# Performance work log

Measured on AMD Instinct MI355X. Metric: run time of the kernel, lower is better.

Reference implementation:

```python
import jax, jax.numpy as jnp
import numpy as np

B, T, D, H, G = 256, 1024, 32, 64, 4 * 64  # batch, seq, input, hidden, gates


def setup_inputs() -> dict:
    key = jax.random.key(0)
    ks = jax.random.split(key, 12)
    s = 1.0 / np.sqrt(H)  # PyTorch LSTM default init scale
    return {
        "x": jax.random.normal(ks[0], (B, T, D), dtype=jnp.float32),
        "w_ih_l0": jax.random.normal(ks[1], (G, D), dtype=jnp.float32) * s,
        "w_hh_l0": jax.random.normal(ks[2], (G, H), dtype=jnp.float32) * s,
        "b_ih_l0": jax.random.normal(ks[3], (G,), dtype=jnp.float32) * s,
        "b_hh_l0": jax.random.normal(ks[4], (G,), dtype=jnp.float32) * s,
        "w_ih_l1": jax.random.normal(ks[5], (G, H), dtype=jnp.float32) * s,
        "w_hh_l1": jax.random.normal(ks[6], (G, H), dtype=jnp.float32) * s,
        "b_ih_l1": jax.random.normal(ks[7], (G,), dtype=jnp.float32) * s,
        "b_hh_l1": jax.random.normal(ks[8], (G,), dtype=jnp.float32) * s,
        "w_fc": jax.random.normal(ks[9], (1, H), dtype=jnp.float32) * s,
        "b_fc": jax.random.normal(ks[10], (1,), dtype=jnp.float32) * s,
    }


def _lstm_layer(x, w_ih, w_hh, b_ih, b_hh):
    """x: [B, T, Din] -> h_seq [B, T, H]. PyTorch gate order (i, f, g, o)."""
    # Precompute input contribution for all timesteps in one GEMM.
    gx = jnp.einsum('btd,gd->btg', x, w_ih) + b_ih + b_hh  # [B, T, 4H]
    gx = jnp.swapaxes(gx, 0, 1)  # [T, B, 4H] for scan over time
    h0 = jnp.zeros((x.shape[0], H), dtype=x.dtype)
    c0 = jnp.zeros((x.shape[0], H), dtype=x.dtype)

    def step(carry, g_t):
        h, c = carry
        g = g_t + h @ w_hh.T  # [B, 4H]
        i, f, gg, o = jnp.split(g, 4, axis=-1)
        i = jax.nn.sigmoid(i)
        f = jax.nn.sigmoid(f)
        gg = jnp.tanh(gg)
        o = jax.nn.sigmoid(o)
        c = f * c + i * gg
        h = o * jnp.tanh(c)
        return (h, c), h

    _, h_seq = jax.lax.scan(step, (h0, c0), gx)  # h_seq: [T, B, H]
    return jnp.swapaxes(h_seq, 0, 1)  # [B, T, H]


def reference(x, w_ih_l0, w_hh_l0, b_ih_l0, b_hh_l0,
              w_ih_l1, w_hh_l1, b_ih_l1, b_hh_l1, w_fc, b_fc):
    h1 = _lstm_layer(x, w_ih_l0, w_hh_l0, b_ih_l0, b_hh_l0)
    h2 = _lstm_layer(h1, w_ih_l1, w_hh_l1, b_ih_l1, b_hh_l1)
    last = h2[:, -1, :]  # [B, H]
    logits = last @ w_fc.T + b_fc  # [B, 1]
    return jax.nn.sigmoid(logits)
```

## Files before the change

kernel.cpp:

```cpp
#include <hip/hip_runtime.h>

#define TT 1024
#define DD 32
#define HH 64

typedef __fp16 h2 __attribute__((ext_vector_type(2)));

__device__ __forceinline__ float fsig(float x) {
    float e = __builtin_amdgcn_exp2f(-1.4426950408889634f * x);
    return __builtin_amdgcn_rcpf(1.0f + e);
}

template<int CTRL>
__device__ __forceinline__ float fdpp(float x) {
    int r = __builtin_amdgcn_mov_dpp(__builtin_bit_cast(int, x), CTRL, 0xf, 0xf, true);
    return __builtin_bit_cast(float, r);
}

struct __attribute__((aligned(16))) H16 { h2 p[8]; };

__device__ __forceinline__ void cvt4rtn(float4 f, h2* d) {
    d[0] = (h2){(__fp16)f.x, (__fp16)f.y};
    d[1] = (h2){(__fp16)f.z, (__fp16)f.w};
}

__global__ __launch_bounds__(512, 1) void lstm2_dot2(
    const float* __restrict__ x,
    const float* __restrict__ w_ih_l0, const float* __restrict__ w_hh_l0,
    const float* __restrict__ b_ih_l0, const float* __restrict__ b_hh_l0,
    const float* __restrict__ w_ih_l1, const float* __restrict__ w_hh_l1,
    const float* __restrict__ b_ih_l1, const float* __restrict__ b_hh_l1,
    const float* __restrict__ w_fc,   const float* __restrict__ b_fc,
    float* __restrict__ out)
{
    const int b    = blockIdx.x;
    const int tid  = threadIdx.x;
    const bool isL1 = tid < 256;
    const int gtid = tid & 255;
    const int q    = gtid & 3;
    const int j    = gtid >> 2;
    const int g    = q * 64 + j;

    __shared__ __attribute__((aligned(32))) __fp16 h1s[2][HH];
    __shared__ __attribute__((aligned(32))) __fp16 h2sB[2][HH];
    if (tid < HH) {
        h1s[0][tid] = (__fp16)0.f; h1s[1][tid] = (__fp16)0.f;
        h2sB[0][tid] = (__fp16)0.f; h2sB[1][tid] = (__fp16)0.f;
    }

    const float kk = (q == 2) ? -2.885390081777927f : -1.4426950408889634f;
    const float aa = (q == 2) ? 2.0f : 1.0f;
    const float bb = (q == 2) ? -1.0f : 0.0f;

    h2 wh[64];
    float bias;
    if (isL1) {
        #pragma unroll
        for (int m = 0; m < 4; ++m) {
            const float4* pih = (const float4*)(w_ih_l0 + (m*64 + j)*DD + q*8);
            cvt4rtn(pih[0], &wh[m*12 + 0]);
            cvt4rtn(pih[1], &wh[m*12 + 2]);
            const float4* phh = (const float4*)(w_hh_l0 + (m*64 + j)*HH + q*16);
            cvt4rtn(phh[0], &wh[m*12 + 4]);
            cvt4rtn(phh[1], &wh[m*12 + 6]);
            cvt4rtn(phh[2], &wh[m*12 + 8]);
            cvt4rtn(phh[3], &wh[m*12 + 10]);
        }
        bias = b_ih_l0[g] + b_hh_l0[g];
    } else {
        #pragma unroll
        for (int m = 0; m < 4; ++m) {
            const float4* pih = (const float4*)(w_ih_l1 + (m*64 + j)*HH + q*16);
            cvt4rtn(pih[0], &wh[m*16 + 0]);
            cvt4rtn(pih[1], &wh[m*16 + 2]);
            cvt4rtn(pih[2], &wh[m*16 + 4]);
            cvt4rtn(pih[3], &wh[m*16 + 6]);
            const float4* phh = (const float4*)(w_hh_l1 + (m*64 + j)*HH + q*16);
            cvt4rtn(phh[0], &wh[m*16 + 8]);
            cvt4rtn(phh[1], &wh[m*16 + 10]);
            cvt4rtn(phh[2], &wh[m*16 + 12]);
            cvt4rtn(phh[3], &wh[m*16 + 14]);
        }
        bias = b_ih_l1[g] + b_hh_l1[g];
    }

    float c = 0.0f;

    const float* xbase = x + (size_t)b * TT * DD + q * 8;
    h2 xh[4];
    if (isL1) {
        const float4* xp = (const float4*)xbase;
        float4 a0 = xp[0], a1 = xp[1];
        xh[0] = __builtin_amdgcn_cvt_pkrtz(a0.x, a0.y);
        xh[1] = __builtin_amdgcn_cvt_pkrtz(a0.z, a0.w);
        xh[2] = __builtin_amdgcn_cvt_pkrtz(a1.x, a1.y);
        xh[3] = __builtin_amdgcn_cvt_pkrtz(a1.z, a1.w);
    }

    __syncthreads();

    for (int t = 0; t <= TT; ++t) {
        const int prev = (t + 1) & 1;
        const int cur  = t & 1;
        if (isL1) {
            if (t < TT) {
                const int tn = (t + 1 < TT) ? (t + 1) : t;
                const float4* xp = (const float4*)(xbase + (size_t)tn * DD);
                float4 n0 = xp[0], n1 = xp[1];

                H16 hq = *(const H16*)&h1s[prev][q*16];

                float P[4];
                #pragma unroll
                for (int m = 0; m < 4; ++m) {
                    float s = 0.0f;
                    #pragma unroll
                    for (int k = 0; k < 4; ++k)
                        s = __builtin_amdgcn_fdot2(wh[m*12 + k], xh[k], s, false);
                    #pragma unroll
                    for (int k = 0; k < 8; ++k)
                        s = __builtin_amdgcn_fdot2(wh[m*12 + 4 + k], hq.p[k], s, false);
                    P[m] = s;
                }

                float t0 = P[0] + fdpp<0xB1>(P[0]);
                float t1 = P[1] + fdpp<0xB1>(P[1]);
                float t2 = P[2] + fdpp<0xB1>(P[2]);
                float t3 = P[3] + fdpp<0xB1>(P[3]);
                float Alo = (q & 1) ? t1 : t0;
                float Ahi = (q & 1) ? t3 : t2;
                float ulo = Alo + fdpp<0x4E>(Alo);
                float uhi = Ahi + fdpp<0x4E>(Ahi);
                float S = ((q & 2) ? uhi : ulo) + bias;

                float e = __builtin_amdgcn_exp2f(kk * S);
                float v = aa * __builtin_amdgcn_rcpf(1.0f + e) + bb;

                float gi = fdpp<0x00>(v);
                float gf = fdpp<0x55>(v);
                float gg = fdpp<0xAA>(v);
                float go = fdpp<0xFF>(v);
                c = gf * c + gi * gg;
                float e2 = __builtin_amdgcn_exp2f(-2.885390081777927f * c);
                float th = 2.0f * __builtin_amdgcn_rcpf(1.0f + e2) - 1.0f;
                float hv = go * th;
                if (q == 0) h1s[cur][j] = (__fp16)hv;

                xh[0] = __builtin_amdgcn_cvt_pkrtz(n0.x, n0.y);
                xh[1] = __builtin_amdgcn_cvt_pkrtz(n0.z, n0.w);
                xh[2] = __builtin_amdgcn_cvt_pkrtz(n1.x, n1.y);
                xh[3] = __builtin_amdgcn_cvt_pkrtz(n1.z, n1.w);
            }
        } else {
            if (t > 0) {
                H16 a1 = *(const H16*)&h1s[prev][q*16];
                H16 a2 = *(const H16*)&h2sB[prev][q*16];

                float P[4];
                #pragma unroll
                for (int m = 0; m < 4; ++m) {
                    float s = 0.0f;
                    #pragma unroll
                    for (int k = 0; k < 8; ++k)
                        s = __builtin_amdgcn_fdot2(wh[m*16 + k], a1.p[k], s, false);
                    #pragma unroll
                    for (int k = 0; k < 8; ++k)
                        s = __builtin_amdgcn_fdot2(wh[m*16 + 8 + k], a2.p[k], s, false);
                    P[m] = s;
                }

                float t0 = P[0] + fdpp<0xB1>(P[0]);
                float t1 = P[1] + fdpp<0xB1>(P[1]);
                float t2 = P[2] + fdpp<0xB1>(P[2]);
                float t3 = P[3] + fdpp<0xB1>(P[3]);
                float Alo = (q & 1) ? t1 : t0;
                float Ahi = (q & 1) ? t3 : t2;
                float ulo = Alo + fdpp<0x4E>(Alo);
                float uhi = Ahi + fdpp<0x4E>(Ahi);
                float S = ((q & 2) ? uhi : ulo) + bias;

                float e = __builtin_amdgcn_exp2f(kk * S);
                float v = aa * __builtin_amdgcn_rcpf(1.0f + e) + bb;

                float gi = fdpp<0x00>(v);
                float gf = fdpp<0x55>(v);
                float gg = fdpp<0xAA>(v);
                float go = fdpp<0xFF>(v);
                c = gf * c + gi * gg;
                float e2 = __builtin_amdgcn_exp2f(-2.885390081777927f * c);
                float th = 2.0f * __builtin_amdgcn_rcpf(1.0f + e2) - 1.0f;
                float hv = go * th;
                if (q == 0) h2sB[cur][j] = (__fp16)hv;
            }
        }
        __syncthreads();
    }

    if (tid < HH) {
        float v = (float)h2sB[0][tid] * w_fc[tid];
        #pragma unroll
        for (int off = 32; off > 0; off >>= 1) v += __shfl_down(v, off);
        if (tid == 0) out[b] = fsig(v + b_fc[0]);
    }
}

extern "C" void kernel_launch(void* const* d_in, const int* in_sizes, int n_in,
                              void* d_out, int out_size, void* d_ws, size_t ws_size,
                              hipStream_t stream) {
    lstm2_dot2<<<dim3(256), dim3(512), 0, stream>>>(
        (const float*)d_in[0],
        (const float*)d_in[1], (const float*)d_in[2],
        (const float*)d_in[3], (const float*)d_in[4],
        (const float*)d_in[5], (const float*)d_in[6],
        (const float*)d_in[7], (const float*)d_in[8],
        (const float*)d_in[9], (const float*)d_in[10],
        (float*)d_out);
}
```

Baseline: 571.0 us.

## Split each gate dot product across eight lanes with 1024-thread blocks

Blocks grow from 512 to 1024 threads, and each hidden unit now uses eight lanes instead of four, each covering half the previous K-chunk. This halves the serial fdot2 chain per timestep in both layers and the per-thread weight registers. An extra ds_swizzle xor-4 step finishes the cross-lane reduction. The aim is to shorten per-step latency in the recurrence, at the cost of a swizzle through the LDS crossbar and a 16-wave barrier every step.

```diff
diff --git a/kernel.cpp b/kernel.cpp
--- a/kernel.cpp
+++ b/kernel.cpp
@@ -17,14 +17,20 @@
     return __builtin_bit_cast(float, r);
 }
 
-struct __attribute__((aligned(16))) H16 { h2 p[8]; };
-
-__device__ __forceinline__ void cvt4rtn(float4 f, h2* d) {
-    d[0] = (h2){(__fp16)f.x, (__fp16)f.y};
-    d[1] = (h2){(__fp16)f.z, (__fp16)f.w};
-}
-
-__global__ __launch_bounds__(512, 1) void lstm2_dot2(
+__device__ __forceinline__ float fswz4(float x) {
+    int r = __builtin_amdgcn_ds_swizzle(__builtin_bit_cast(int, x), 0x101F);
+    return __builtin_bit_cast(float, r);
+}
+
+struct __attribute__((aligned(16))) H8 { h2 p[4]; };
+
+__device__ __forceinline__ void cvt4(float4 f, h2* d) {
+    d[0] = __builtin_amdgcn_cvt_pkrtz(f.x, f.y);
+    d[1] = __builtin_amdgcn_cvt_pkrtz(f.z, f.w);
+}
+
+__global__ __launch_bounds__(1024) __attribute__((amdgpu_waves_per_eu(4, 4)))
+void lstm2_w16(
     const float* __restrict__ x,
     const float* __restrict__ w_ih_l0, const float* __restrict__ w_hh_l0,
     const float* __restrict__ b_ih_l0, const float* __restrict__ b_hh_l0,
@@ -35,11 +41,11 @@
 {
     const int b    = blockIdx.x;
     const int tid  = threadIdx.x;
-    const bool isL1 = tid < 256;
-    const int gtid = tid & 255;
-    const int q    = gtid & 3;
-    const int j    = gtid >> 2;
-    const int g    = q * 64 + j;
+    const bool isL1 = tid < 512;
+    const int gtid = tid & 511;
+    const int c_ch = gtid & 7;
+    const int j    = gtid >> 3;
+    const int ga   = (c_ch & 3) * 64 + j;
 
     __shared__ __attribute__((aligned(32))) __fp16 h1s[2][HH];
     __shared__ __attribute__((aligned(32))) __fp16 h2sB[2][HH];
@@ -48,53 +54,43 @@
         h2sB[0][tid] = (__fp16)0.f; h2sB[1][tid] = (__fp16)0.f;
     }
 
-    const float kk = (q == 2) ? -2.885390081777927f : -1.4426950408889634f;
-    const float aa = (q == 2) ? 2.0f : 1.0f;
-    const float bb = (q == 2) ? -1.0f : 0.0f;
-
-    h2 wh[64];
+    const float kk = ((c_ch & 3) == 2) ? -2.885390081777927f : -1.4426950408889634f;
+    const float aa = ((c_ch & 3) == 2) ? 2.0f : 1.0f;
+    const float bb = ((c_ch & 3) == 2) ? -1.0f : 0.0f;
+
+    h2 wh[32];
     float bias;
     if (isL1) {
         #pragma unroll
         for (int m = 0; m < 4; ++m) {
-            const float4* pih = (const float4*)(w_ih_l0 + (m*64 + j)*DD + q*8);
-            cvt4rtn(pih[0], &wh[m*12 + 0]);
-            cvt4rtn(pih[1], &wh[m*12 + 2]);
-            const float4* phh = (const float4*)(w_hh_l0 + (m*64 + j)*HH + q*16);
-            cvt4rtn(phh[0], &wh[m*12 + 4]);
-            cvt4rtn(phh[1], &wh[m*12 + 6]);
-            cvt4rtn(phh[2], &wh[m*12 + 8]);
-            cvt4rtn(phh[3], &wh[m*12 + 10]);
+            float4 fih = *(const float4*)(w_ih_l0 + (m*64 + j)*DD + c_ch*4);
+            cvt4(fih, &wh[m*6 + 0]);
+            const float4* phh = (const float4*)(w_hh_l0 + (m*64 + j)*HH + c_ch*8);
+            cvt4(phh[0], &wh[m*6 + 2]);
+            cvt4(phh[1], &wh[m*6 + 4]);
         }
-        bias = b_ih_l0[g] + b_hh_l0[g];
+        bias = b_ih_l0[ga] + b_hh_l0[ga];
     } else {
         #pragma unroll
         for (int m = 0; m < 4; ++m) {
-            const float4* pih = (const float4*)(w_ih_l1 + (m*64 + j)*HH + q*16);
-            cvt4rtn(pih[0], &wh[m*16 + 0]);
-            cvt4rtn(pih[1], &wh[m*16 + 2]);
-            cvt4rtn(pih[2], &wh[m*16 + 4]);
-            cvt4rtn(pih[3], &wh[m*16 + 6]);
-            const float4* phh = (const float4*)(w_hh_l1 + (m*64 + j)*HH + q*16);
-            cvt4rtn(phh[0], &wh[m*16 + 8]);
-            cvt4rtn(phh[1], &wh[m*16 + 10]);
-            cvt4rtn(phh[2], &wh[m*16 + 12]);
-            cvt4rtn(phh[3], &wh[m*16 + 14]);
+            const float4* pih = (const float4*)(w_ih_l1 + (m*64 + j)*HH + c_ch*8);
+            cvt4(pih[0], &wh[m*8 + 0]);
+            cvt4(pih[1], &wh[m*8 + 2]);
+            const float4* phh = (const float4*)(w_hh_l1 + (m*64 + j)*HH + c_ch*8);
+            cvt4(phh[0], &wh[m*8 + 4]);
+            cvt4(phh[1], &wh[m*8 + 6]);
         }
-        bias = b_ih_l1[g] + b_hh_l1[g];
-    }
-
-    float c = 0.0f;
-
-    const float* xbase = x + (size_t)b * TT * DD + q * 8;
-    h2 xh[4];
+        bias = b_ih_l1[ga] + b_hh_l1[ga];
+    }
+
+    float cst = 0.0f;
+
+    const float* xbase = x + (size_t)b * TT * DD + c_ch * 4;
+    h2 xh[2];
     if (isL1) {
-        const float4* xp = (const float4*)xbase;
-        float4 a0 = xp[0], a1 = xp[1];
+        float4 a0 = *(const float4*)xbase;
         xh[0] = __builtin_amdgcn_cvt_pkrtz(a0.x, a0.y);
         xh[1] = __builtin_amdgcn_cvt_pkrtz(a0.z, a0.w);
-        xh[2] = __builtin_amdgcn_cvt_pkrtz(a1.x, a1.y);
-        xh[3] = __builtin_amdgcn_cvt_pkrtz(a1.z, a1.w);
     }
 
     __syncthreads();
@@ -105,10 +101,53 @@
         if (isL1) {
             if (t < TT) {
                 const int tn = (t + 1 < TT) ? (t + 1) : t;
-                const float4* xp = (const float4*)(xbase + (size_t)tn * DD);
-                float4 n0 = xp[0], n1 = xp[1];
-
-                H16 hq = *(const H16*)&h1s[prev][q*16];
+                float4 n0 = *(const float4*)(xbase + (size_t)tn * DD);
+
+                H8 hq = *(const H8*)&h1s[prev][c_ch*8];
+
+                float P[4];
+                #pragma unroll
+                for (int m = 0; m < 4; ++m) {
+                    float s = 0.0f;
+                    s = __builtin_amdgcn_fdot2(wh[m*6 + 0], xh[0], s, false);
+                    s = __builtin_amdgcn_fdot2(wh[m*6 + 1], xh[1], s, false);
+                    #pragma unroll
+                    for (int k = 0; k < 4; ++k)
+                        s = __builtin_amdgcn_fdot2(wh[m*6 + 2 + k], hq.p[k], s, false);
+                    P[m] = s;
+                }
+
+                float t0 = P[0] + fdpp<0xB1>(P[0]);
+                float t1 = P[1] + fdpp<0xB1>(P[1]);
+                float t2 = P[2] + fdpp<0xB1>(P[2]);
+                float t3 = P[3] + fdpp<0xB1>(P[3]);
+                float Alo = (c_ch & 1) ? t1 : t0;
+                float Ahi = (c_ch & 1) ? t3 : t2;
+                float ulo = Alo + fdpp<0x4E>(Alo);
+                float uhi = Ahi + fdpp<0x4E>(Ahi);
+                float Sh = (c_ch & 2) ? uhi : ulo;
+                float S = Sh + fswz4(Sh) + bias;
+
+                float e = __builtin_amdgcn_exp2f(kk * S);
+                float v = aa * __builtin_amdgcn_rcpf(1.0f + e) + bb;
+
+                float gi = fdpp<0x00>(v);
+                float gf = fdpp<0x55>(v);
+                float gg = fdpp<0xAA>(v);
+                float go = fdpp<0xFF>(v);
+                cst = gf * cst + gi * gg;
+                float e2 = __builtin_amdgcn_exp2f(-2.885390081777927f * cst);
+                float th = 2.0f * __builtin_amdgcn_rcpf(1.0f + e2) - 1.0f;
+                float hv = go * th;
+                if (c_ch == 0) h1s[cur][j] = (__fp16)hv;
+
+                xh[0] = __builtin_amdgcn_cvt_pkrtz(n0.x, n0.y);
+                xh[1] = __builtin_amdgcn_cvt_pkrtz(n0.z, n0.w);
+            }
+        } else {
+            if (t > 0) {
+                H8 a1 = *(const H8*)&h1s[prev][c_ch*8];
+                H8 a2 = *(const H8*)&h2sB[prev][c_ch*8];
 
                 float P[4];
                 #pragma unroll
@@ -116,10 +155,10 @@
                     float s = 0.0f;
                     #pragma unroll
                     for (int k = 0; k < 4; ++k)
-                        s = __builtin_amdgcn_fdot2(wh[m*12 + k], xh[k], s, false);
+                        s = __builtin_amdgcn_fdot2(wh[m*8 + k], a1.p[k], s, false);
                     #pragma unroll
-                    for (int k = 0; k < 8; ++k)
-                        s = __builtin_amdgcn_fdot2(wh[m*12 + 4 + k], hq.p[k], s, false);
+                    for (int k = 0; k < 4; ++k)
+                        s = __builtin_amdgcn_fdot2(wh[m*8 + 4 + k], a2.p[k], s, false);
                     P[m] = s;
                 }
 
@@ -127,11 +166,12 @@
                 float t1 = P[1] + fdpp<0xB1>(P[1]);
                 float t2 = P[2] + fdpp<0xB1>(P[2]);
                 float t3 = P[3] + fdpp<0xB1>(P[3]);
-                float Alo = (q & 1) ? t1 : t0;
-                float Ahi = (q & 1) ? t3 : t2;
+                float Alo = (c_ch & 1) ? t1 : t0;
+                float Ahi = (c_ch & 1) ? t3 : t2;
                 float ulo = Alo + fdpp<0x4E>(Alo);
                 float uhi = Ahi + fdpp<0x4E>(Ahi);
-                float S = ((q & 2) ? uhi : ulo) + bias;
+                float Sh = (c_ch & 2) ? uhi : ulo;
+                float S = Sh + fswz4(Sh) + bias;
 
                 float e = __builtin_amdgcn_exp2f(kk * S);
                 float v = aa * __builtin_amdgcn_rcpf(1.0f + e) + bb;
@@ -140,57 +180,11 @@
                 float gf = fdpp<0x55>(v);
                 float gg = fdpp<0xAA>(v);
                 float go = fdpp<0xFF>(v);
-                c = gf * c + gi * gg;
-                float e2 = __builtin_amdgcn_exp2f(-2.885390081777927f * c);
+                cst = gf * cst + gi * gg;
+                float e2 = __builtin_amdgcn_exp2f(-2.885390081777927f * cst);
                 float th = 2.0f * __builtin_amdgcn_rcpf(1.0f + e2) - 1.0f;
                 float hv = go * th;
-                if (q == 0) h1s[cur][j] = (__fp16)hv;
-
-                xh[0] = __builtin_amdgcn_cvt_pkrtz(n0.x, n0.y);
-                xh[1] = __builtin_amdgcn_cvt_pkrtz(n0.z, n0.w);
-                xh[2] = __builtin_amdgcn_cvt_pkrtz(n1.x, n1.y);
-                xh[3] = __builtin_amdgcn_cvt_pkrtz(n1.z, n1.w);
-            }
-        } else {
-            if (t > 0) {
-                H16 a1 = *(const H16*)&h1s[prev][q*16];
-                H16 a2 = *(const H16*)&h2sB[prev][q*16];
-
-                float P[4];
-                #pragma unroll
-                for (int m = 0; m < 4; ++m) {
-                    float s = 0.0f;
-                    #pragma unroll
-                    for (int k = 0; k < 8; ++k)
-                        s = __builtin_amdgcn_fdot2(wh[m*16 + k], a1.p[k], s, false);
-                    #pragma unroll
-                    for (int k = 0; k < 8; ++k)
-                        s = __builtin_amdgcn_fdot2(wh[m*16 + 8 + k], a2.p[k], s, false);
-                    P[m] = s;
-                }
-
-                float t0 = P[0] + fdpp<0xB1>(P[0]);
-                float t1 = P[1] + fdpp<0xB1>(P[1]);
-                float t2 = P[2] + fdpp<0xB1>(P[2]);
-                float t3 = P[3] + fdpp<0xB1>(P[3]);
-                float Alo = (q & 1) ? t1 : t0;
-                float Ahi = (q & 1) ? t3 : t2;
-                float ulo = Alo + fdpp<0x4E>(Alo);
-                float uhi = Ahi + fdpp<0x4E>(Ahi);
-                float S = ((q & 2) ? uhi : ulo) + bias;
-
-                float e = __builtin_amdgcn_exp2f(kk * S);
-                float v = aa * __builtin_amdgcn_rcpf(1.0f + e) + bb;
-
-                float gi = fdpp<0x00>(v);
-                float gf = fdpp<0x55>(v);
-                float gg = fdpp<0xAA>(v);
-                float go = fdpp<0xFF>(v);
-                c = gf * c + gi * gg;
-                float e2 = __builtin_amdgcn_exp2f(-2.885390081777927f * c);
-                float th = 2.0f * __builtin_amdgcn_rcpf(1.0f + e2) - 1.0f;
-                float hv = go * th;
-                if (q == 0) h2sB[cur][j] = (__fp16)hv;
+                if (c_ch == 0) h2sB[cur][j] = (__fp16)hv;
             }
         }
         __syncthreads();
@@ -207,7 +201,7 @@
 extern "C" void kernel_launch(void* const* d_in, const int* in_sizes, int n_in,
                               void* d_out, int out_size, void* d_ws, size_t ws_size,
                               hipStream_t stream) {
-    lstm2_dot2<<<dim3(256), dim3(512), 0, stream>>>(
+    lstm2_w16<<<dim3(256), dim3(1024), 0, stream>>>(
         (const float*)d_in[0],
         (const float*)d_in[1], (const float*)d_in[2],
         (const float*)d_in[3], (const float*)d_in[4],
```

Result: slower. 742.6 us (+30.1%).

## Precompute layer-0 input gates in separate kernel and re-split recurrent work

Applied to the files above, without the earlier changes.

Adds a kernel that computes the layer-0 input projection plus biases for all timesteps into an fp16 workspace. The recurrent kernel then loads one precomputed value per gate per step instead of doing the x dot products. Layer-1 moves to 512 threads with two threads per gate, so each block has 768 threads and the per-step cross-lane reductions get shorter. The cost is a 128MB round trip through memory and an extra launch, and the fused kernel is kept as a fallback when the workspace is too small.

```diff
diff --git a/kernel.cpp b/kernel.cpp
--- a/kernel.cpp
+++ b/kernel.cpp
@@ -17,14 +17,212 @@
     return __builtin_bit_cast(float, r);
 }
 
+__device__ __forceinline__ float fswz4(float x) {
+    int r = __builtin_amdgcn_ds_swizzle(__builtin_bit_cast(int, x), 0x101F);
+    return __builtin_bit_cast(float, r);
+}
+
 struct __attribute__((aligned(16))) H16 { h2 p[8]; };
 
-__device__ __forceinline__ void cvt4rtn(float4 f, h2* d) {
-    d[0] = (h2){(__fp16)f.x, (__fp16)f.y};
-    d[1] = (h2){(__fp16)f.z, (__fp16)f.w};
-}
-
-__global__ __launch_bounds__(512, 1) void lstm2_dot2(
+__device__ __forceinline__ h2 pk(float a, float b) {
+    return __builtin_amdgcn_cvt_pkrtz(a, b);
+}
+
+__global__ __launch_bounds__(256) void gx_precompute(
+    const float* __restrict__ x, const float* __restrict__ w_ih_l0,
+    const float* __restrict__ b_ih_l0, const float* __restrict__ b_hh_l0,
+    __fp16* __restrict__ gx)
+{
+    const int blk = blockIdx.x;
+    const int b   = blk >> 4;
+    const int tq  = blk & 15;
+    const int tid = threadIdx.x;
+    const int q   = tid & 3;
+    const int j   = tid >> 2;
+    const int g   = q * 64 + j;
+
+    __shared__ __attribute__((aligned(16))) h2 xlds[512];
+
+    h2 wk[16];
+    {
+        const float4* wp = (const float4*)(w_ih_l0 + g * DD);
+        #pragma unroll
+        for (int i = 0; i < 8; ++i) {
+            float4 f = wp[i];
+            wk[2*i]   = pk(f.x, f.y);
+            wk[2*i+1] = pk(f.z, f.w);
+        }
+    }
+    const float bias = b_ih_l0[g] + b_hh_l0[g];
+
+    const float* xb = x + (size_t)b * (TT*DD) + tq * 64 * DD;
+    __fp16* gxo = gx + ((size_t)b * TT + tq * 64) * 256 + tid;
+
+    #pragma unroll
+    for (int sc = 0; sc < 2; ++sc) {
+        __syncthreads();
+        {
+            float4 f = *(const float4*)(xb + sc * 1024 + tid * 4);
+            xlds[tid*2]   = pk(f.x, f.y);
+            xlds[tid*2+1] = pk(f.z, f.w);
+        }
+        __syncthreads();
+        for (int tl = 0; tl < 32; ++tl) {
+            H16 xa = *(const H16*)&xlds[tl*16];
+            H16 xb2 = *(const H16*)&xlds[tl*16 + 8];
+            float s0 = 0.f, s1 = 0.f;
+            #pragma unroll
+            for (int k = 0; k < 8; ++k) s0 = __builtin_amdgcn_fdot2(wk[k],   xa.p[k],  s0, false);
+            #pragma unroll
+            for (int k = 0; k < 8; ++k) s1 = __builtin_amdgcn_fdot2(wk[8+k], xb2.p[k], s1, false);
+            gxo[(sc*32 + tl) * 256] = (__fp16)(s0 + s1 + bias);
+        }
+    }
+}
+
+__global__ __launch_bounds__(768, 3) void lstm2_pre(
+    const float* __restrict__ w_hh_l0,
+    const float* __restrict__ w_ih_l1, const float* __restrict__ w_hh_l1,
+    const float* __restrict__ b_ih_l1, const float* __restrict__ b_hh_l1,
+    const float* __restrict__ w_fc,   const float* __restrict__ b_fc,
+    const __fp16* __restrict__ gx,
+    float* __restrict__ out)
+{
+    const int b    = blockIdx.x;
+    const int tid  = threadIdx.x;
+    const bool isL1 = tid < 256;
+    const int lid  = isL1 ? tid : (tid - 256);
+    const int q    = lid & 3;
+    const int jL1  = lid >> 2;
+    const int m    = lid & 3;
+    const int half = (lid >> 2) & 1;
+    const int jL2  = lid >> 3;
+
+    __shared__ __attribute__((aligned(32))) __fp16 h1s[2][HH];
+    __shared__ __attribute__((aligned(32))) __fp16 h2sB[2][HH];
+    if (tid < HH) {
+        h1s[0][tid] = (__fp16)0.f; h1s[1][tid] = (__fp16)0.f;
+        h2sB[0][tid] = (__fp16)0.f; h2sB[1][tid] = (__fp16)0.f;
+    }
+
+    const int gsel = isL1 ? q : m;
+    const float kk = (gsel == 2) ? -2.885390081777927f : -1.4426950408889634f;
+    const float aa = (gsel == 2) ? 2.0f : 1.0f;
+    const float bb = (gsel == 2) ? -1.0f : 0.0f;
+
+    h2 wh[32];
+    float bias = 0.f;
+    if (isL1) {
+        const float4* wp = (const float4*)(w_hh_l0 + (q*64 + jL1) * HH);
+        #pragma unroll
+        for (int i = 0; i < 16; ++i) {
+            float4 f = wp[i];
+            wh[2*i]   = pk(f.x, f.y);
+            wh[2*i+1] = pk(f.z, f.w);
+        }
+    } else {
+        const float* wrow = (half == 0) ? (w_ih_l1 + (m*64 + jL2) * HH)
+                                        : (w_hh_l1 + (m*64 + jL2) * HH);
+        const float4* wp = (const float4*)wrow;
+        #pragma unroll
+        for (int i = 0; i < 16; ++i) {
+            float4 f = wp[i];
+            wh[2*i]   = pk(f.x, f.y);
+            wh[2*i+1] = pk(f.z, f.w);
+        }
+        bias = b_ih_l1[m*64 + jL2] + b_hh_l1[m*64 + jL2];
+    }
+
+    float c = 0.0f;
+
+    const __fp16* gxp = gx + ((size_t)b << 18) + lid;
+    float gxv = isL1 ? (float)gxp[0] : 0.f;
+
+    __syncthreads();
+
+    for (int t = 0; t <= TT; ++t) {
+        const int prev = (t + 1) & 1;
+        const int cur  = t & 1;
+        if (isL1) {
+            if (t < TT) {
+                const int tn = (t + 1 < TT) ? (t + 1) : t;
+                float gnext = (float)gxp[(size_t)tn << 8];
+
+                H16 hA = *(const H16*)&h1s[prev][0];
+                H16 hB = *(const H16*)&h1s[prev][16];
+                H16 hC = *(const H16*)&h1s[prev][32];
+                H16 hD = *(const H16*)&h1s[prev][48];
+
+                float s0 = gxv, s1 = 0.f, s2 = 0.f, s3 = 0.f;
+                #pragma unroll
+                for (int k = 0; k < 8; ++k) {
+                    s0 = __builtin_amdgcn_fdot2(wh[k],      hA.p[k], s0, false);
+                    s1 = __builtin_amdgcn_fdot2(wh[8 + k],  hB.p[k], s1, false);
+                    s2 = __builtin_amdgcn_fdot2(wh[16 + k], hC.p[k], s2, false);
+                    s3 = __builtin_amdgcn_fdot2(wh[24 + k], hD.p[k], s3, false);
+                }
+                float S = (s0 + s1) + (s2 + s3);
+
+                float e = __builtin_amdgcn_exp2f(kk * S);
+                float v = aa * __builtin_amdgcn_rcpf(1.0f + e) + bb;
+
+                float gi = fdpp<0x00>(v);
+                float gf = fdpp<0x55>(v);
+                float gg = fdpp<0xAA>(v);
+                float go = fdpp<0xFF>(v);
+                c = gf * c + gi * gg;
+                float e2 = __builtin_amdgcn_exp2f(-2.885390081777927f * c);
+                float th = 2.0f * __builtin_amdgcn_rcpf(1.0f + e2) - 1.0f;
+                float hv = go * th;
+                if (q == 0) h1s[cur][jL1] = (__fp16)hv;
+
+                gxv = gnext;
+            }
+        } else {
+            if (t > 0) {
+                const __fp16* hsrc = half ? &h2sB[prev][0] : &h1s[prev][0];
+                H16 hA = *(const H16*)&hsrc[0];
+                H16 hB = *(const H16*)&hsrc[16];
+                H16 hC = *(const H16*)&hsrc[32];
+                H16 hD = *(const H16*)&hsrc[48];
+
+                float s0 = 0.f, s1 = 0.f, s2 = 0.f, s3 = 0.f;
+                #pragma unroll
+                for (int k = 0; k < 8; ++k) {
+                    s0 = __builtin_amdgcn_fdot2(wh[k],      hA.p[k], s0, false);
+                    s1 = __builtin_amdgcn_fdot2(wh[8 + k],  hB.p[k], s1, false);
+                    s2 = __builtin_amdgcn_fdot2(wh[16 + k], hC.p[k], s2, false);
+                    s3 = __builtin_amdgcn_fdot2(wh[24 + k], hD.p[k], s3, false);
+                }
+                float Sp = (s0 + s1) + (s2 + s3);
+                float S = Sp + fswz4(Sp) + bias;
+
+                float e = __builtin_amdgcn_exp2f(kk * S);
+                float v = aa * __builtin_amdgcn_rcpf(1.0f + e) + bb;
+
+                float gi = fdpp<0x00>(v);
+                float gf = fdpp<0x55>(v);
+                float gg = fdpp<0xAA>(v);
+                float go = fdpp<0xFF>(v);
+                c = gf * c + gi * gg;
+                float e2 = __builtin_amdgcn_exp2f(-2.885390081777927f * c);
+                float th = 2.0f * __builtin_amdgcn_rcpf(1.0f + e2) - 1.0f;
+                float hv = go * th;
+                if ((lid & 7) == 0) h2sB[cur][jL2] = (__fp16)hv;
+            }
+        }
+        __syncthreads();
+    }
+
+    if (tid < HH) {
+        float v = (float)h2sB[0][tid] * w_fc[tid];
+        #pragma unroll
+        for (int off = 32; off > 0; off >>= 1) v += __shfl_down(v, off);
+        if (tid == 0) out[b] = fsig(v + b_fc[0]);
+    }
+}
+
+__global__ __launch_bounds__(512) void lstm2_fb(
     const float* __restrict__ x,
     const float* __restrict__ w_ih_l0, const float* __restrict__ w_hh_l0,
     const float* __restrict__ b_ih_l0, const float* __restrict__ b_hh_l0,
@@ -47,7 +245,6 @@
         h1s[0][tid] = (__fp16)0.f; h1s[1][tid] = (__fp16)0.f;
         h2sB[0][tid] = (__fp16)0.f; h2sB[1][tid] = (__fp16)0.f;
     }
-
     const float kk = (q == 2) ? -2.885390081777927f : -1.4426950408889634f;
     const float aa = (q == 2) ? 2.0f : 1.0f;
     const float bb = (q == 2) ? -1.0f : 0.0f;
@@ -56,47 +253,50 @@
     float bias;
     if (isL1) {
         #pragma unroll
-        for (int m = 0; m < 4; ++m) {
-            const float4* pih = (const float4*)(w_ih_l0 + (m*64 + j)*DD + q*8);
-            cvt4rtn(pih[0], &wh[m*12 + 0]);
-            cvt4rtn(pih[1], &wh[m*12 + 2]);
-            const float4* phh = (const float4*)(w_hh_l0 + (m*64 + j)*HH + q*16);
-            cvt4rtn(phh[0], &wh[m*12 + 4]);
-            cvt4rtn(phh[1], &wh[m*12 + 6]);
-            cvt4rtn(phh[2], &wh[m*12 + 8]);
-            cvt4rtn(phh[3], &wh[m*12 + 10]);
+        for (int mm = 0; mm < 4; ++mm) {
+            const float4* pih = (const float4*)(w_ih_l0 + (mm*64 + j)*DD + q*8);
+            float4 f0 = pih[0], f1 = pih[1];
+            wh[mm*12+0] = pk(f0.x,f0.y); wh[mm*12+1] = pk(f0.z,f0.w);
+            wh[mm*12+2] = pk(f1.x,f1.y); wh[mm*12+3] = pk(f1.z,f1.w);
+            const float4* phh = (const float4*)(w_hh_l0 + (mm*64 + j)*HH + q*16);
+            #pragma unroll
+            for (int i = 0; i < 4; ++i) {
+                float4 f = phh[i];
+                wh[mm*12+4+2*i]   = pk(f.x,f.y);
+                wh[mm*12+4+2*i+1] = pk(f.z,f.w);
+            }
         }
         bias = b_ih_l0[g] + b_hh_l0[g];
     } else {
         #pragma unroll
-        for (int m = 0; m < 4; ++m) {
-            const float4* pih = (const float4*)(w_ih_l1 + (m*64 + j)*HH + q*16);
-            cvt4rtn(pih[0], &wh[m*16 + 0]);
-            cvt4rtn(pih[1], &wh[m*16 + 2]);
-            cvt4rtn(pih[2], &wh[m*16 + 4]);
-            cvt4rtn(pih[3], &wh[m*16 + 6]);
-            const float4* phh = (const float4*)(w_hh_l1 + (m*64 + j)*HH + q*16);
-            cvt4rtn(phh[0], &wh[m*16 + 8]);
-            cvt4rtn(phh[1], &wh[m*16 + 10]);
-            cvt4rtn(phh[2], &wh[m*16 + 12]);
-            cvt4rtn(phh[3], &wh[m*16 + 14]);
+        for (int mm = 0; mm < 4; ++mm) {
+            const float4* pih = (const float4*)(w_ih_l1 + (mm*64 + j)*HH + q*16);
+            const float4* phh = (const float4*)(w_hh_l1 + (mm*64 + j)*HH + q*16);
+            #pragma unroll
+            for (int i = 0; i < 4; ++i) {
+                float4 f = pih[i];
+                wh[mm*16+2*i]   = pk(f.x,f.y);
+                wh[mm*16+2*i+1] = pk(f.z,f.w);
+            }
+            #pragma unroll
+            for (int i = 0; i < 4; ++i) {
+                float4 f = phh[i];
+                wh[mm*16+8+2*i]   = pk(f.x,f.y);
+                wh[mm*16+8+2*i+1] = pk(f.z,f.w);
+            }
         }
         bias = b_ih_l1[g] + b_hh_l1[g];
     }
 
     float c = 0.0f;
-
     const float* xbase = x + (size_t)b * TT * DD + q * 8;
     h2 xh[4];
     if (isL1) {
         const float4* xp = (const float4*)xbase;
         float4 a0 = xp[0], a1 = xp[1];
-        xh[0] = __builtin_amdgcn_cvt_pkrtz(a0.x, a0.y);
-        xh[1] = __builtin_amdgcn_cvt_pkrtz(a0.z, a0.w);
-        xh[2] = __builtin_amdgcn_cvt_pkrtz(a1.x, a1.y);
-        xh[3] = __builtin_amdgcn_cvt_pkrtz(a1.z, a1.w);
-    }
-
+        xh[0] = pk(a0.x,a0.y); xh[1] = pk(a0.z,a0.w);
+        xh[2] = pk(a1.x,a1.y); xh[3] = pk(a1.z,a1.w);
+    }
     __syncthreads();
 
     for (int t = 0; t <= TT; ++t) {
@@ -107,22 +307,19 @@
                 const int tn = (t + 1 < TT) ? (t + 1) : t;
                 const float4* xp = (const float4*)(xbase + (size_t)tn * DD);
                 float4 n0 = xp[0], n1 = xp[1];
-
                 H16 hq = *(const H16*)&h1s[prev][q*16];
-
                 float P[4];
                 #pragma unroll
-                for (int m = 0; m < 4; ++m) {
+                for (int mm = 0; mm < 4; ++mm) {
                     float s = 0.0f;
                     #pragma unroll
                     for (int k = 0; k < 4; ++k)
-                        s = __builtin_amdgcn_fdot2(wh[m*12 + k], xh[k], s, false);
+                        s = __builtin_amdgcn_fdot2(wh[mm*12 + k], xh[k], s, false);
                     #pragma unroll
                     for (int k = 0; k < 8; ++k)
-                        s = __builtin_amdgcn_fdot2(wh[m*12 + 4 + k], hq.p[k], s, false);
-                    P[m] = s;
+                        s = __builtin_amdgcn_fdot2(wh[mm*12 + 4 + k], hq.p[k], s, false);
+                    P[mm] = s;
                 }
-
                 float t0 = P[0] + fdpp<0xB1>(P[0]);
                 float t1 = P[1] + fdpp<0xB1>(P[1]);
                 float t2 = P[2] + fdpp<0xB1>(P[2]);
@@ -132,10 +329,8 @@
                 float ulo = Alo + fdpp<0x4E>(Alo);
                 float uhi = Ahi + fdpp<0x4E>(Ahi);
                 float S = ((q & 2) ? uhi : ulo) + bias;
-
                 float e = __builtin_amdgcn_exp2f(kk * S);
                 float v = aa * __builtin_amdgcn_rcpf(1.0f + e) + bb;
-
                 float gi = fdpp<0x00>(v);
                 float gf = fdpp<0x55>(v);
                 float gg = fdpp<0xAA>(v);
@@ -145,30 +340,25 @@
                 float th = 2.0f * __builtin_amdgcn_rcpf(1.0f + e2) - 1.0f;
                 float hv = go * th;
                 if (q == 0) h1s[cur][j] = (__fp16)hv;
-
-                xh[0] = __builtin_amdgcn_cvt_pkrtz(n0.x, n0.y);
-                xh[1] = __builtin_amdgcn_cvt_pkrtz(n0.z, n0.w);
-                xh[2] = __builtin_amdgcn_cvt_pkrtz(n1.x, n1.y);
-                xh[3] = __builtin_amdgcn_cvt_pkrtz(n1.z, n1.w);
+                xh[0] = pk(n0.x,n0.y); xh[1] = pk(n0.z,n0.w);
+                xh[2] = pk(n1.x,n1.y); xh[3] = pk(n1.z,n1.w);
             }
         } else {
             if (t > 0) {
                 H16 a1 = *(const H16*)&h1s[prev][q*16];
                 H16 a2 = *(const H16*)&h2sB[prev][q*16];
-
                 float P[4];
                 #pragma unroll
-                for (int m = 0; m < 4; ++m) {
+                for (int mm = 0; mm < 4; ++mm) {
                     float s = 0.0f;
                     #pragma unroll
                     for (int k = 0; k < 8; ++k)
-                        s = __builtin_amdgcn_fdot2(wh[m*16 + k], a1.p[k], s, false);
+                        s = __builtin_amdgcn_fdot2(wh[mm*16 + k], a1.p[k], s, false);
                     #pragma unroll
                     for (int k = 0; k < 8; ++k)
-                        s = __builtin_amdgcn_fdot2(wh[m*16 + 8 + k], a2.p[k], s, false);
-                    P[m] = s;
+                        s = __builtin_amdgcn_fdot2(wh[mm*16 + 8 + k], a2.p[k], s, false);
+                    P[mm] = s;
                 }
-
                 float t0 = P[0] + fdpp<0xB1>(P[0]);
                 float t1 = P[1] + fdpp<0xB1>(P[1]);
                 float t2 = P[2] + fdpp<0xB1>(P[2]);
@@ -178,10 +368,8 @@
                 float ulo = Alo + fdpp<0x4E>(Alo);
                 float uhi = Ahi + fdpp<0x4E>(Ahi);
                 float S = ((q & 2) ? uhi : ulo) + bias;
-
                 float e = __builtin_amdgcn_exp2f(kk * S);
                 float v = aa * __builtin_amdgcn_rcpf(1.0f + e) + bb;
-
                 float gi = fdpp<0x00>(v);
                 float gf = fdpp<0x55>(v);
                 float gg = fdpp<0xAA>(v);
@@ -207,12 +395,26 @@
 extern "C" void kernel_launch(void* const* d_in, const int* in_sizes, int n_in,
                               void* d_out, int out_size, void* d_ws, size_t ws_size,
                               hipStream_t stream) {
-    lstm2_dot2<<<dim3(256), dim3(512), 0, stream>>>(
-        (const float*)d_in[0],
-        (const float*)d_in[1], (const float*)d_in[2],
-        (const float*)d_in[3], (const float*)d_in[4],
-        (const float*)d_in[5], (const float*)d_in[6],
-        (const float*)d_in[7], (const float*)d_in[8],
-        (const float*)d_in[9], (const float*)d_in[10],
-        (float*)d_out);
-}
+    const size_t gx_bytes = (size_t)256 * TT * 256 * sizeof(__fp16);
+    if (ws_size >= gx_bytes) {
+        __fp16* gx = (__fp16*)d_ws;
+        gx_precompute<<<dim3(256 * 16), dim3(256), 0, stream>>>(
+            (const float*)d_in[0], (const float*)d_in[1],
+            (const float*)d_in[3], (const float*)d_in[4], gx);
+        lstm2_pre<<<dim3(256), dim3(768), 0, stream>>>(
+            (const float*)d_in[2],
+            (const float*)d_in[5], (const float*)d_in[6],
+            (const float*)d_in[7], (const float*)d_in[8],
+            (const float*)d_in[9], (const float*)d_in[10],
+            gx, (float*)d_out);
+    } else {
+        lstm2_fb<<<dim3(256), dim3(512), 0, stream>>>(
+            (const float*)d_in[0],
+            (const float*)d_in[1], (const float*)d_in[2],
+            (const float*)d_in[3], (const float*)d_in[4],
+            (const float*)d_in[5], (const float*)d_in[6],
+            (const float*)d_in[7], (const float*)d_in[8],
+            (const float*)d_in[9], (const float*)d_in[10],
+            (float*)d_out);
+    }
+}
```

Result: slower. 703.3 us (+23.2%).

## Precompute layer-0 input gates in separate kernel and rotate recurrent dot products

Applied to the files above, without the earlier changes.

Adds a pre-pass kernel that computes the layer-0 input projection plus biases for all timesteps into an fp16 workspace, removing that work from the serial recurrence. The recurrent kernel grows to 768 threads: each layer-0 thread owns a full gate row, and layer-1 splits each gate over two threads (input and hidden halves), combined with a swizzle. Weights are stored in a per-lane rotated order over a duplicated hidden-state buffer to avoid LDS bank conflicts, and the DPP cross-lane reductions are removed. This trades more threads and an extra global read per step, plus a pre-pass, for a shorter per-step critical path.

```diff
diff --git a/kernel.cpp b/kernel.cpp
--- a/kernel.cpp
+++ b/kernel.cpp
@@ -17,85 +17,127 @@
     return __builtin_bit_cast(float, r);
 }
 
-struct __attribute__((aligned(16))) H16 { h2 p[8]; };
-
-__device__ __forceinline__ void cvt4rtn(float4 f, h2* d) {
-    d[0] = (h2){(__fp16)f.x, (__fp16)f.y};
-    d[1] = (h2){(__fp16)f.z, (__fp16)f.w};
-}
-
-__global__ __launch_bounds__(512, 1) void lstm2_dot2(
-    const float* __restrict__ x,
-    const float* __restrict__ w_ih_l0, const float* __restrict__ w_hh_l0,
+__device__ __forceinline__ float fswz4(float x) {
+    int r = __builtin_amdgcn_ds_swizzle(__builtin_bit_cast(int, x), 0x101F);
+    return __builtin_bit_cast(float, r);
+}
+
+struct __attribute__((aligned(16))) H8 { h2 p[4]; };
+
+__device__ __forceinline__ h2 pk(float a, float b) {
+    return __builtin_amdgcn_cvt_pkrtz(a, b);
+}
+
+__device__ __forceinline__ void vdot(float& s, h2 w, h2 h) {
+    asm("v_dot2_f32_f16 %0, %1, %2, %0" : "+v"(s) : "v"(w), "v"(h));
+}
+
+__global__ __launch_bounds__(256) void gx_precompute(
+    const float* __restrict__ x, const float* __restrict__ w_ih_l0,
     const float* __restrict__ b_ih_l0, const float* __restrict__ b_hh_l0,
+    __fp16* __restrict__ gx)
+{
+    const int blk = blockIdx.x;
+    const int b   = blk >> 4;
+    const int tq  = blk & 15;
+    const int tid = threadIdx.x;
+    const int q   = tid & 3;
+    const int j   = tid >> 2;
+    const int g   = q * 64 + j;
+
+    __shared__ __attribute__((aligned(16))) h2 xlds[512];
+
+    h2 wk[16];
+    {
+        const float4* wp = (const float4*)(w_ih_l0 + g * DD);
+        #pragma unroll
+        for (int i = 0; i < 8; ++i) {
+            float4 f = wp[i];
+            wk[2*i]   = pk(f.x, f.y);
+            wk[2*i+1] = pk(f.z, f.w);
+        }
+    }
+    const float bias = b_ih_l0[g] + b_hh_l0[g];
+
+    const float* xb = x + (size_t)b * (TT*DD) + tq * 64 * DD;
+    __fp16* gxo = gx + ((size_t)b * TT + tq * 64) * 256 + tid;
+
+    #pragma unroll
+    for (int sc = 0; sc < 2; ++sc) {
+        __syncthreads();
+        {
+            float4 f = *(const float4*)(xb + sc * 1024 + tid * 4);
+            xlds[tid*2]   = pk(f.x, f.y);
+            xlds[tid*2+1] = pk(f.z, f.w);
+        }
+        __syncthreads();
+        for (int tl = 0; tl < 32; ++tl) {
+            float s0 = 0.f, s1 = 0.f;
+            #pragma unroll
+            for (int k = 0; k < 8; ++k) s0 = __builtin_amdgcn_fdot2(wk[k],   xlds[tl*16 + k],     s0, false);
+            #pragma unroll
+            for (int k = 0; k < 8; ++k) s1 = __builtin_amdgcn_fdot2(wk[8+k], xlds[tl*16 + 8 + k], s1, false);
+            gxo[(sc*32 + tl) * 256] = (__fp16)(s0 + s1 + bias);
+        }
+    }
+}
+
+__global__ __launch_bounds__(768) void lstm2_rot(
+    const float* __restrict__ w_hh_l0,
     const float* __restrict__ w_ih_l1, const float* __restrict__ w_hh_l1,
     const float* __restrict__ b_ih_l1, const float* __restrict__ b_hh_l1,
     const float* __restrict__ w_fc,   const float* __restrict__ b_fc,
+    const __fp16* __restrict__ gx,
     float* __restrict__ out)
 {
     const int b    = blockIdx.x;
     const int tid  = threadIdx.x;
     const bool isL1 = tid < 256;
-    const int gtid = tid & 255;
-    const int q    = gtid & 3;
-    const int j    = gtid >> 2;
-    const int g    = q * 64 + j;
-
-    __shared__ __attribute__((aligned(32))) __fp16 h1s[2][HH];
-    __shared__ __attribute__((aligned(32))) __fp16 h2sB[2][HH];
-    if (tid < HH) {
+    const int lid  = isL1 ? tid : (tid - 256);
+    const int q    = lid & 3;
+    const int jL1  = lid >> 2;
+    const int half = (lid >> 2) & 1;
+    const int jL2  = lid >> 3;
+    const int r    = lid & 7;
+
+    __shared__ __attribute__((aligned(16))) __fp16 h1s[2][128];
+    __shared__ __attribute__((aligned(16))) __fp16 h2s[2][128];
+    if (tid < 128) {
         h1s[0][tid] = (__fp16)0.f; h1s[1][tid] = (__fp16)0.f;
-        h2sB[0][tid] = (__fp16)0.f; h2sB[1][tid] = (__fp16)0.f;
+        h2s[0][tid] = (__fp16)0.f; h2s[1][tid] = (__fp16)0.f;
     }
 
     const float kk = (q == 2) ? -2.885390081777927f : -1.4426950408889634f;
     const float aa = (q == 2) ? 2.0f : 1.0f;
     const float bb = (q == 2) ? -1.0f : 0.0f;
 
-    h2 wh[64];
-    float bias;
-    if (isL1) {
+    h2 wh[32];
+    float bias = 0.f;
+    {
+        const float* wrow;
+        if (isL1) {
+            wrow = w_hh_l0 + (q*64 + jL1) * HH;
+        } else {
+            const int g2 = q*64 + jL2;
+            wrow = half ? (w_hh_l1 + g2 * HH) : (w_ih_l1 + g2 * HH);
+            bias = b_ih_l1[g2] + b_hh_l1[g2];
+        }
         #pragma unroll
-        for (int m = 0; m < 4; ++m) {
-            const float4* pih = (const float4*)(w_ih_l0 + (m*64 + j)*DD + q*8);
-            cvt4rtn(pih[0], &wh[m*12 + 0]);
-            cvt4rtn(pih[1], &wh[m*12 + 2]);
-            const float4* phh = (const float4*)(w_hh_l0 + (m*64 + j)*HH + q*16);
-            cvt4rtn(phh[0], &wh[m*12 + 4]);
-            cvt4rtn(phh[1], &wh[m*12 + 6]);
-            cvt4rtn(phh[2], &wh[m*12 + 8]);
-            cvt4rtn(phh[3], &wh[m*12 + 10]);
-        }
-        bias = b_ih_l0[g] + b_hh_l0[g];
-    } else {
-        #pragma unroll
-        for (int m = 0; m < 4; ++m) {
-            const float4* pih = (const float4*)(w_ih_l1 + (m*64 + j)*HH + q*16);
-            cvt4rtn(pih[0], &wh[m*16 + 0]);
-            cvt4rtn(pih[1], &wh[m*16 + 2]);
-            cvt4rtn(pih[2], &wh[m*16 + 4]);
-            cvt4rtn(pih[3], &wh[m*16 + 6]);
-            const float4* phh = (const float4*)(w_hh_l1 + (m*64 + j)*HH + q*16);
-            cvt4rtn(phh[0], &wh[m*16 + 8]);
-            cvt4rtn(phh[1], &wh[m*16 + 10]);
-            cvt4rtn(phh[2], &wh[m*16 + 12]);
-            cvt4rtn(phh[3], &wh[m*16 + 14]);
-        }
-        bias = b_ih_l1[g] + b_hh_l1[g];
+        for (int i = 0; i < 8; ++i) {
+            const int c = (i + r) & 7;
+            float4 f0 = *(const float4*)(wrow + c*8);
+            float4 f1 = *(const float4*)(wrow + c*8 + 4);
+            wh[4*i+0] = pk(f0.x, f0.y);
+            wh[4*i+1] = pk(f0.z, f0.w);
+            wh[4*i+2] = pk(f1.x, f1.y);
+            wh[4*i+3] = pk(f1.z, f1.w);
+        }
     }
 
     float c = 0.0f;
 
-    const float* xbase = x + (size_t)b * TT * DD + q * 8;
-    h2 xh[4];
-    if (isL1) {
-        const float4* xp = (const float4*)xbase;
-        float4 a0 = xp[0], a1 = xp[1];
-        xh[0] = __builtin_amdgcn_cvt_pkrtz(a0.x, a0.y);
-        xh[1] = __builtin_amdgcn_cvt_pkrtz(a0.z, a0.w);
-        xh[2] = __builtin_amdgcn_cvt_pkrtz(a1.x, a1.y);
-        xh[3] = __builtin_amdgcn_cvt_pkrtz(a1.z, a1.w);
-    }
+    const __fp16* gxp = gx + ((size_t)b << 18) + lid;
+    float gxv = isL1 ? (float)gxp[0] : 0.f;
 
     __syncthreads();
 
@@ -105,33 +147,27 @@
         if (isL1) {
             if (t < TT) {
                 const int tn = (t + 1 < TT) ? (t + 1) : t;
-                const float4* xp = (const float4*)(xbase + (size_t)tn * DD);
-                float4 n0 = xp[0], n1 = xp[1];
-
-                H16 hq = *(const H16*)&h1s[prev][q*16];
-
-                float P[4];
-                #pragma unroll
-                for (int m = 0; m < 4; ++m) {
-                    float s = 0.0f;
-                    #pragma unroll
-                    for (int k = 0; k < 4; ++k)
-                        s = __builtin_amdgcn_fdot2(wh[m*12 + k], xh[k], s, false);
-                    #pragma unroll
-                    for (int k = 0; k < 8; ++k)
-                        s = __builtin_amdgcn_fdot2(wh[m*12 + 4 + k], hq.p[k], s, false);
-                    P[m] = s;
-                }
-
-                float t0 = P[0] + fdpp<0xB1>(P[0]);
-                float t1 = P[1] + fdpp<0xB1>(P[1]);
-                float t2 = P[2] + fdpp<0xB1>(P[2]);
-                float t3 = P[3] + fdpp<0xB1>(P[3]);
-                float Alo = (q & 1) ? t1 : t0;
-                float Ahi = (q & 1) ? t3 : t2;
-                float ulo = Alo + fdpp<0x4E>(Alo);
-                float uhi = Ahi + fdpp<0x4E>(Ahi);
-                float S = ((q & 2) ? uhi : ulo) + bias;
+                float gnext = (float)gxp[(size_t)tn << 8];
+
+                const H8* hc = (const H8*)&h1s[prev][0];
+                H8 c0 = hc[r+0], c1 = hc[r+1], c2 = hc[r+2], c3 = hc[r+3];
+                float p0 = gxv, p1 = 0.f, p2 = 0.f, p3 = 0.f;
+                #pragma unroll
+                for (int k = 0; k < 4; ++k) {
+                    vdot(p0, wh[k],      c0.p[k]);
+                    vdot(p1, wh[4 + k],  c1.p[k]);
+                    vdot(p2, wh[8 + k],  c2.p[k]);
+                    vdot(p3, wh[12 + k], c3.p[k]);
+                }
+                H8 c4 = hc[r+4], c5 = hc[r+5], c6 = hc[r+6], c7 = hc[r+7];
+                #pragma unroll
+                for (int k = 0; k < 4; ++k) {
+                    vdot(p0, wh[16 + k], c4.p[k]);
+                    vdot(p1, wh[20 + k], c5.p[k]);
+                    vdot(p2, wh[24 + k], c6.p[k]);
+                    vdot(p3, wh[28 + k], c7.p[k]);
+                }
+                float S = (p0 + p1) + (p2 + p3);
 
                 float e = __builtin_amdgcn_exp2f(kk * S);
                 float v = aa * __builtin_amdgcn_rcpf(1.0f + e) + bb;
@@ -144,40 +180,36 @@
                 float e2 = __builtin_amdgcn_exp2f(-2.885390081777927f * c);
                 float th = 2.0f * __builtin_amdgcn_rcpf(1.0f + e2) - 1.0f;
                 float hv = go * th;
-                if (q == 0) h1s[cur][j] = (__fp16)hv;
-
-                xh[0] = __builtin_amdgcn_cvt_pkrtz(n0.x, n0.y);
-                xh[1] = __builtin_amdgcn_cvt_pkrtz(n0.z, n0.w);
-                xh[2] = __builtin_amdgcn_cvt_pkrtz(n1.x, n1.y);
-                xh[3] = __builtin_amdgcn_cvt_pkrtz(n1.z, n1.w);
+                if (q == 0) {
+                    __fp16 hv16 = (__fp16)hv;
+                    h1s[cur][jL1]      = hv16;
+                    h1s[cur][64 + jL1] = hv16;
+                }
+                gxv = gnext;
             }
         } else {
             if (t > 0) {
-                H16 a1 = *(const H16*)&h1s[prev][q*16];
-                H16 a2 = *(const H16*)&h2sB[prev][q*16];
-
-                float P[4];
-                #pragma unroll
-                for (int m = 0; m < 4; ++m) {
-                    float s = 0.0f;
-                    #pragma unroll
-                    for (int k = 0; k < 8; ++k)
-                        s = __builtin_amdgcn_fdot2(wh[m*16 + k], a1.p[k], s, false);
-                    #pragma unroll
-                    for (int k = 0; k < 8; ++k)
-                        s = __builtin_amdgcn_fdot2(wh[m*16 + 8 + k], a2.p[k], s, false);
-                    P[m] = s;
-                }
-
-                float t0 = P[0] + fdpp<0xB1>(P[0]);
-                float t1 = P[1] + fdpp<0xB1>(P[1]);
-                float t2 = P[2] + fdpp<0xB1>(P[2]);
-                float t3 = P[3] + fdpp<0xB1>(P[3]);
-                float Alo = (q & 1) ? t1 : t0;
-                float Ahi = (q & 1) ? t3 : t2;
-                float ulo = Alo + fdpp<0x4E>(Alo);
-                float uhi = Ahi + fdpp<0x4E>(Ahi);
-                float S = ((q & 2) ? uhi : ulo) + bias;
+                const H8* hc = half ? (const H8*)&h2s[prev][0]
+                                    : (const H8*)&h1s[prev][0];
+                H8 c0 = hc[r+0], c1 = hc[r+1], c2 = hc[r+2], c3 = hc[r+3];
+                float p0 = 0.f, p1 = 0.f, p2 = 0.f, p3 = 0.f;
+                #pragma unroll
+                for (int k = 0; k < 4; ++k) {
+                    vdot(p0, wh[k],      c0.p[k]);
+                    vdot(p1, wh[4 + k],  c1.p[k]);
+                    vdot(p2, wh[8 + k],  c2.p[k]);
+                    vdot(p3, wh[12 + k], c3.p[k]);
+                }
+                H8 c4 = hc[r+4], c5 = hc[r+5], c6 = hc[r+6], c7 = hc[r+7];
+                #pragma unroll
+                for (int k = 0; k < 4; ++k) {
+                    vdot(p0, wh[16 + k], c4.p[k]);
+                    vdot(p1, wh[20 + k], c5.p[k]);
+                    vdot(p2, wh[24 + k], c6.p[k]);
+                    vdot(p3, wh[28 + k], c7.p[k]);
+                }
+                float Sp = (p0 + p1) + (p2 + p3);
+                float S = Sp + fswz4(Sp) + bias;
 
                 float e = __builtin_amdgcn_exp2f(kk * S);
                 float v = aa * __builtin_amdgcn_rcpf(1.0f + e) + bb;
@@ -190,14 +222,18 @@
                 float e2 = __builtin_amdgcn_exp2f(-2.885390081777927f * c);
                 float th = 2.0f * __builtin_amdgcn_rcpf(1.0f + e2) - 1.0f;
                 float hv = go * th;
-                if (q == 0) h2sB[cur][j] = (__fp16)hv;
+                if ((lid & 7) == 0) {
+                    __fp16 hv16 = (__fp16)hv;
+                    h2s[cur][jL2]      = hv16;
+                    h2s[cur][64 + jL2] = hv16;
+                }
             }
         }
         __syncthreads();
     }
 
     if (tid < HH) {
-        float v = (float)h2sB[0][tid] * w_fc[tid];
+        float v = (float)h2s[0][tid] * w_fc[tid];
         #pragma unroll
         for (int off = 32; off > 0; off >>= 1) v += __shfl_down(v, off);
         if (tid == 0) out[b] = fsig(v + b_fc[0]);
@@ -207,12 +243,14 @@
 extern "C" void kernel_launch(void* const* d_in, const int* in_sizes, int n_in,
                               void* d_out, int out_size, void* d_ws, size_t ws_size,
                               hipStream_t stream) {
-    lstm2_dot2<<<dim3(256), dim3(512), 0, stream>>>(
-        (const float*)d_in[0],
-        (const float*)d_in[1], (const float*)d_in[2],
-        (const float*)d_in[3], (const float*)d_in[4],
+    __fp16* gx = (__fp16*)d_ws;
+    gx_precompute<<<dim3(256 * 16), dim3(256), 0, stream>>>(
+        (const float*)d_in[0], (const float*)d_in[1],
+        (const float*)d_in[3], (const float*)d_in[4], gx);
+    lstm2_rot<<<dim3(256), dim3(768), 0, stream>>>(
+        (const float*)d_in[2],
         (const float*)d_in[5], (const float*)d_in[6],
         (const float*)d_in[7], (const float*)d_in[8],
         (const float*)d_in[9], (const float*)d_in[10],
-        (float*)d_out);
-}
+        gx, (float*)d_out);
+}
```

New measurement: 702.2 us. 23.0% more time.
